# Optimization experiments

Measured on AMD Instinct MI355X. Metric: run time of the kernel, lower is better.

Reference implementation:

```python
import jax, jax.numpy as jnp
import numpy as np

B, S, D, H, E, K, F = 1, 1024, 1024, 16, 8, 2, 4096


def setup_inputs() -> dict:
    key = jax.random.key(0)
    ks = jax.random.split(key, 8)
    n = lambda k, shape, sc: (jax.random.normal(k, shape, dtype=jnp.float32) * sc)
    return {
        "x": n(ks[0], (B, S, D), 1.0),
        "w_qkv": n(ks[1], (D, 3 * D), D ** -0.5),
        "w_o": n(ks[2], (D, D), D ** -0.5),
        "g1": jnp.ones((D,), jnp.float32),
        "b1": jnp.zeros((D,), jnp.float32),
        "wg": n(ks[3], (D, E), D ** -0.5),
        "w1": n(ks[4], (E, D, F), D ** -0.5),
        "bb1": jnp.zeros((E, F), jnp.float32),
        "w2": n(ks[5], (E, F, D), F ** -0.5),
        "bb2": jnp.zeros((E, D), jnp.float32),
        "g2": jnp.ones((D,), jnp.float32),
        "b2": jnp.zeros((D,), jnp.float32),
    }


def layernorm(x, g, b, eps=1e-5):
    m = x.mean(-1, keepdims=True)
    v = ((x - m) ** 2).mean(-1, keepdims=True)
    return (x - m) * jax.lax.rsqrt(v + eps) * g + b


def reference(x, w_qkv, w_o, g1, b1, wg, w1, bb1, w2, bb2, g2, b2):
    b, s, d = x.shape
    hd = d // H
    # --- multi-head causal self-attention ---
    qkv = x @ w_qkv  # [b,s,3d]
    q, k, v = jnp.split(qkv, 3, axis=-1)
    to_heads = lambda t: t.reshape(b, s, H, hd).transpose(0, 2, 1, 3)  # [b,h,s,hd]
    q, k, v = to_heads(q), to_heads(k), to_heads(v)
    scores = jnp.einsum("bhqd,bhkd->bhqk", q, k) / jnp.sqrt(jnp.float32(hd))
    causal = jnp.tril(jnp.ones((s, s), bool))
    scores = jnp.where(causal, scores, jnp.finfo(scores.dtype).min)
    attn = jax.nn.softmax(scores, axis=-1)
    o = jnp.einsum("bhqk,bhkd->bhqd", attn, v)
    o = o.transpose(0, 2, 1, 3).reshape(b, s, d) @ w_o
    # --- add & norm ---
    h = layernorm(x + o, g1, b1)
    # --- MoE FFN: softmax router, top-k, renormalized combine ---
    probs = jax.nn.softmax(h @ wg, axis=-1)  # [b,s,E]
    topv, topi = jax.lax.top_k(probs, K)
    topv = topv / topv.sum(-1, keepdims=True)
    w = (topv[..., None] * jax.nn.one_hot(topi, E, dtype=h.dtype)).sum(-2)  # [b,s,E]
    h1 = jax.nn.gelu(jnp.einsum("bsd,edf->ebsf", h, w1) + bb1[:, None, None, :])
    y = jnp.einsum("ebsf,efd->ebsd", h1, w2) + bb2[:, None, None, :]
    moe = jnp.einsum("ebsd,bse->bsd", y, w)
    # --- residual + norm of MoE block ---
    return layernorm(h + moe, g2, b2)
```

## Files before the change

kernel.cpp:

```cpp
#include <hip/hip_runtime.h>
#include <hip/hip_bf16.h>
#include <math.h>

#define SEQ 1024
#define DIM 1024
#define NH  16
#define NE  8
#define FF  4096

typedef float f32x4 __attribute__((ext_vector_type(4)));
typedef short short8 __attribute__((ext_vector_type(8)));
typedef short s16x4 __attribute__((ext_vector_type(4)));

#define WAIT_VM(N) asm volatile("s_waitcnt vmcnt(" #N ")" ::: "memory")

__device__ __forceinline__ ushort f2bf(float f) {
  union { float f; unsigned u; } v; v.f = f;
  unsigned r = v.u + 0x7FFF + ((v.u >> 16) & 1);
  return (ushort)(r >> 16);
}
__device__ __forceinline__ float bf2f(ushort h) {
  union { unsigned u; float f; } v; v.u = ((unsigned)h) << 16;
  return v.f;
}

__device__ __forceinline__ float gelu_tanh(float x) {
  return 0.5f * x * (1.f + tanhf(0.7978845608028654f * (x + 0.044715f * x * x * x)));
}
__device__ __forceinline__ float gelu_fast(float x) {
  float u = 1.5957691216057308f * (x + 0.044715f * x * x * x);
  return x / (1.f + __expf(-u));
}

__device__ __forceinline__ void gl2lds16(const void* g, void* l) {
  __builtin_amdgcn_global_load_lds(
      (const __attribute__((address_space(1))) unsigned int*)g,
      (__attribute__((address_space(3))) unsigned int*)l, 16, 0, 0);
}

__global__ __launch_bounds__(256) void wconv_kernel(
    const float* __restrict__ w1, const float* __restrict__ w2,
    const float* __restrict__ wq, const float* __restrict__ wo,
    ushort* __restrict__ w1T, ushort* __restrict__ w2T,
    ushort* __restrict__ wqT, ushort* __restrict__ wqTl,
    ushort* __restrict__ woT, ushort* __restrict__ woTl) {
  __shared__ __align__(16) ushort th[64 * 64];
  __shared__ __align__(16) ushort tl[64 * 64];
  int z = blockIdx.z, t = threadIdx.x;
  const float* src; ushort* dh; ushort* dl = nullptr; int R, C, r0, c0;
  if (z < 8) {
    src = w1 + (size_t)z * DIM * FF;  dh = w1T + (size_t)z * FF * DIM;
    R = DIM; C = FF; r0 = blockIdx.y * 64; c0 = blockIdx.x * 64;
  } else if (z < 16) {
    src = w2 + (size_t)(z - 8) * FF * DIM;  dh = w2T + (size_t)(z - 8) * DIM * FF;
    R = FF; C = DIM; r0 = blockIdx.x * 64; c0 = blockIdx.y * 64;
  } else if (z == 16) {
    if (blockIdx.x >= 48) return;
    src = wq; dh = wqT; dl = wqTl;
    R = DIM; C = 3 * DIM; r0 = blockIdx.y * 64; c0 = blockIdx.x * 64;
  } else {
    if (blockIdx.x >= 16) return;
    src = wo; dh = woT; dl = woTl;
    R = DIM; C = DIM; r0 = blockIdx.y * 64; c0 = blockIdx.x * 64;
  }
  int ry = (t >> 4) * 4;
  int cx = (t & 15) * 4;
  f32x4 v[4];
#pragma unroll
  for (int j = 0; j < 4; j++)
    v[j] = *(const f32x4*)&src[(size_t)(r0 + ry + j) * C + c0 + cx];
#pragma unroll
  for (int i = 0; i < 4; i++) {
    int trow = cx + i;
    int o = trow * 64 + (((ry >> 3) ^ (trow & 7)) << 3) + (ry & 7);
    ushort uh[4], ul[4];
#pragma unroll
    for (int j = 0; j < 4; j++) {
      float f = v[j][i];
      ushort hh = f2bf(f);
      uh[j] = hh;
      if (dl) ul[j] = f2bf(f - bf2f(hh));
    }
    *(s16x4*)&th[o] = *(const s16x4*)uh;
    if (dl) *(s16x4*)&tl[o] = *(const s16x4*)ul;
  }
  __syncthreads();
  int tr = t >> 2, tc = (t & 3) * 16;
  int b0 = (tc >> 3) ^ (tr & 7);
  int b1 = ((tc >> 3) + 1) ^ (tr & 7);
  short8 u0 = *(const short8*)&th[tr * 64 + b0 * 8];
  short8 u1 = *(const short8*)&th[tr * 64 + b1 * 8];
  size_t dbase = (size_t)(c0 + tr) * R + r0 + tc;
  *(short8*)&dh[dbase] = u0;
  *(short8*)&dh[dbase + 8] = u1;
  if (dl) {
    short8 l0 = *(const short8*)&tl[tr * 64 + b0 * 8];
    short8 l1 = *(const short8*)&tl[tr * 64 + b1 * 8];
    *(short8*)&dl[dbase] = l0;
    *(short8*)&dl[dbase + 8] = l1;
  }
}

__global__ __launch_bounds__(256) void bfsplit_kernel(const float* __restrict__ in,
                                                      ushort* __restrict__ oh,
                                                      ushort* __restrict__ ol) {
  int i = (blockIdx.x * 256 + threadIdx.x) * 4;
  f32x4 v = *(const f32x4*)&in[i];
  ushort h[4], l[4];
#pragma unroll
  for (int j = 0; j < 4; j++) { h[j] = f2bf(v[j]); l[j] = f2bf(v[j] - bf2f(h[j])); }
  *(s16x4*)&oh[i] = *(const s16x4*)h;
  *(s16x4*)&ol[i] = *(const s16x4*)l;
}

template <int EPI, int KSPLIT>
__global__ __launch_bounds__(256) void mm_fast(
    const ushort* __restrict__ A, const ushort* __restrict__ BT,
    const float* __restrict__ bias, void* __restrict__ Cout,
    const int* __restrict__ tok, const int* __restrict__ offcnt,
    int N, int K)
{
  int zz = blockIdx.z;
  int e  = (KSPLIT > 1) ? (zz & (NE - 1)) : zz;
  int ks = (KSPLIT > 1) ? (zz >> 3) : 0;
  int off = offcnt[e], cnt = offcnt[NE + e];
  int m0 = blockIdx.y * 128;
  if (m0 >= cnt) return;
  int n0 = blockIdx.x * 128;
  const ushort* Bp = BT + (size_t)e * N * K;
  const int Kc = K / KSPLIT;
  const int kbase = ks * Kc;

  __shared__ __align__(16) ushort As[2][128 * 32];
  __shared__ __align__(16) ushort Bs[2][128 * 32];

  int t = threadIdx.x, lane = t & 63, w = t >> 6, wr = w >> 1, wc = w & 1;

  const ushort* aG[2]; const ushort* bG[2];
  int lofs[2];
#pragma unroll
  for (int c = 0; c < 2; c++) {
    int gid = w * 128 + c * 64 + lane;
    int m = gid >> 2, p = gid & 3;
    int kg = p ^ ((m >> 1) & 3);
    int mc = m0 + m; if (mc > cnt - 1) mc = cnt - 1;
    int arow = tok ? tok[off + mc] : (off + mc);
    aG[c] = A + (size_t)arow * K + kbase + kg * 8;
    bG[c] = Bp + (size_t)(n0 + m) * K + kbase + kg * 8;
    lofs[c] = (w * 128 + c * 64) * 8;
  }

  int aro[4], bro[4];
#pragma unroll
  for (int mi = 0; mi < 4; mi++) {
    int m = wr * 64 + mi * 16 + (lane & 15);
    aro[mi] = (m * 4 + ((lane >> 4) ^ ((m >> 1) & 3))) * 8;
  }
#pragma unroll
  for (int ni = 0; ni < 4; ni++) {
    int n = wc * 64 + ni * 16 + (lane & 15);
    bro[ni] = (n * 4 + ((lane >> 4) ^ ((n >> 1) & 3))) * 8;
  }

  f32x4 acc[4][4] = {};
  const int nt = Kc / 32;

#pragma unroll
  for (int c = 0; c < 2; c++) { gl2lds16(aG[c], &As[0][lofs[c]]); gl2lds16(bG[c], &Bs[0][lofs[c]]); }
  if (nt > 1) {
#pragma unroll
    for (int c = 0; c < 2; c++) { gl2lds16(aG[c] + 32, &As[1][lofs[c]]); gl2lds16(bG[c] + 32, &Bs[1][lofs[c]]); }
  }

  for (int tt = 0; tt < nt; tt++) {
    if (tt + 1 < nt) WAIT_VM(4); else WAIT_VM(0);
    __builtin_amdgcn_s_barrier();
    int b = tt & 1;
    short8 af[4], bf[4];
#pragma unroll
    for (int mi = 0; mi < 4; mi++) af[mi] = *(const short8*)&As[b][aro[mi]];
#pragma unroll
    for (int ni = 0; ni < 4; ni++) bf[ni] = *(const short8*)&Bs[b][bro[ni]];
#pragma unroll
    for (int mi = 0; mi < 4; mi++)
#pragma unroll
      for (int ni = 0; ni < 4; ni++)
        acc[mi][ni] = __builtin_amdgcn_mfma_f32_16x16x32_bf16(af[mi], bf[ni], acc[mi][ni], 0, 0, 0);
    asm volatile("s_waitcnt lgkmcnt(0)" ::: "memory");
    __builtin_amdgcn_sched_barrier(0);
    __builtin_amdgcn_s_barrier();
    if (tt + 2 < nt) {
      int ko = (tt + 2) * 32;
#pragma unroll
      for (int c = 0; c < 2; c++) { gl2lds16(aG[c] + ko, &As[b][lofs[c]]); gl2lds16(bG[c] + ko, &Bs[b][lofs[c]]); }
    }
  }

  const float* biasp = (EPI == 3) ? nullptr : bias + (size_t)e * N;
  float* Cp = (float*)Cout + (size_t)ks * 2048 * N;
#pragma unroll
  for (int mi = 0; mi < 4; mi++) {
#pragma unroll
    for (int j = 0; j < 4; j++) {
      int grow = m0 + wr * 64 + mi * 16 + (lane >> 4) * 4 + j;
      if (grow >= cnt) continue;
      size_t rbase = (size_t)(off + grow) * N;
#pragma unroll
      for (int ni = 0; ni < 4; ni++) {
        int gcol = n0 + wc * 64 + ni * 16 + (lane & 15);
        float v = acc[mi][ni][j];
        if (EPI == 1) ((ushort*)Cout)[rbase + gcol] = f2bf(gelu_fast(v + biasp[gcol]));
        else if (EPI == 2) ((float*)Cout)[rbase + gcol] = v + biasp[gcol];
        else Cp[rbase + gcol] = v;
      }
    }
  }
}

__global__ __launch_bounds__(256) void mm_split(
    const ushort* __restrict__ Ah, const ushort* __restrict__ Al,
    const ushort* __restrict__ Bh, const ushort* __restrict__ Bl,
    float* __restrict__ C, int N, int K)
{
  int m0 = blockIdx.y * 128;
  int n0 = blockIdx.x * 128;

  __shared__ __align__(16) ushort Ahs[2][4096], Als[2][4096];
  __shared__ __align__(16) ushort Bhs[2][4096], Bls[2][4096];

  int t = threadIdx.x, lane = t & 63, w = t >> 6, wr = w >> 1, wc = w & 1;

  const ushort *aGh[2], *aGl[2], *bGh[2], *bGl[2];
  int lofs[2];
#pragma unroll
  for (int c = 0; c < 2; c++) {
    int gid = w * 128 + c * 64 + lane;
    int m = gid >> 2, p = gid & 3;
    int kg = p ^ ((m >> 1) & 3);
    aGh[c] = Ah + (size_t)(m0 + m) * K + kg * 8;
    aGl[c] = Al + (size_t)(m0 + m) * K + kg * 8;
    bGh[c] = Bh + (size_t)(n0 + m) * K + kg * 8;
    bGl[c] = Bl + (size_t)(n0 + m) * K + kg * 8;
    lofs[c] = (w * 128 + c * 64) * 8;
  }

  int aro[4], bro[4];
#pragma unroll
  for (int mi = 0; mi < 4; mi++) {
    int m = wr * 64 + mi * 16 + (lane & 15);
    aro[mi] = (m * 4 + ((lane >> 4) ^ ((m >> 1) & 3))) * 8;
  }
#pragma unroll
  for (int ni = 0; ni < 4; ni++) {
    int n = wc * 64 + ni * 16 + (lane & 15);
    bro[ni] = (n * 4 + ((lane >> 4) ^ ((n >> 1) & 3))) * 8;
  }

  f32x4 acc[4][4] = {};
  const int nt = K / 32;

#pragma unroll
  for (int c = 0; c < 2; c++) {
    gl2lds16(aGh[c], &Ahs[0][lofs[c]]); gl2lds16(aGl[c], &Als[0][lofs[c]]);
    gl2lds16(bGh[c], &Bhs[0][lofs[c]]); gl2lds16(bGl[c], &Bls[0][lofs[c]]);
  }
  if (nt > 1) {
#pragma unroll
    for (int c = 0; c < 2; c++) {
      gl2lds16(aGh[c] + 32, &Ahs[1][lofs[c]]); gl2lds16(aGl[c] + 32, &Als[1][lofs[c]]);
      gl2lds16(bGh[c] + 32, &Bhs[1][lofs[c]]); gl2lds16(bGl[c] + 32, &Bls[1][lofs[c]]);
    }
  }

  for (int tt = 0; tt < nt; tt++) {
    if (tt + 1 < nt) WAIT_VM(8); else WAIT_VM(0);
    __builtin_amdgcn_s_barrier();
    int b = tt & 1;
    short8 ah[4], al_[4], bh[4], bl_[4];
#pragma unroll
    for (int mi = 0; mi < 4; mi++) {
      ah[mi] = *(const short8*)&Ahs[b][aro[mi]];
      al_[mi] = *(const short8*)&Als[b][aro[mi]];
    }
#pragma unroll
    for (int ni = 0; ni < 4; ni++) {
      bh[ni] = *(const short8*)&Bhs[b][bro[ni]];
      bl_[ni] = *(const short8*)&Bls[b][bro[ni]];
    }
#pragma unroll
    for (int mi = 0; mi < 4; mi++)
#pragma unroll
      for (int ni = 0; ni < 4; ni++) {
        acc[mi][ni] = __builtin_amdgcn_mfma_f32_16x16x32_bf16(al_[mi], bh[ni], acc[mi][ni], 0, 0, 0);
        acc[mi][ni] = __builtin_amdgcn_mfma_f32_16x16x32_bf16(ah[mi], bl_[ni], acc[mi][ni], 0, 0, 0);
        acc[mi][ni] = __builtin_amdgcn_mfma_f32_16x16x32_bf16(ah[mi], bh[ni], acc[mi][ni], 0, 0, 0);
      }
    asm volatile("s_waitcnt lgkmcnt(0)" ::: "memory");
    __builtin_amdgcn_sched_barrier(0);
    __builtin_amdgcn_s_barrier();
    if (tt + 2 < nt) {
      int ko = (tt + 2) * 32;
#pragma unroll
      for (int c = 0; c < 2; c++) {
        gl2lds16(aGh[c] + ko, &Ahs[b][lofs[c]]); gl2lds16(aGl[c] + ko, &Als[b][lofs[c]]);
        gl2lds16(bGh[c] + ko, &Bhs[b][lofs[c]]); gl2lds16(bGl[c] + ko, &Bls[b][lofs[c]]);
      }
    }
  }

#pragma unroll
  for (int mi = 0; mi < 4; mi++)
#pragma unroll
    for (int j = 0; j < 4; j++) {
      int grow = m0 + wr * 64 + mi * 16 + (lane >> 4) * 4 + j;
      size_t rbase = (size_t)grow * N;
#pragma unroll
      for (int ni = 0; ni < 4; ni++) {
        int gcol = n0 + wc * 64 + ni * 16 + (lane & 15);
        C[rbase + gcol] = acc[mi][ni][j];
      }
    }
}

template <int EPI, int SPLIT>
__global__ __launch_bounds__(256) void mm_bf16(
    const float* __restrict__ A, const float* __restrict__ B,
    const float* __restrict__ bias, float* __restrict__ C,
    const int* __restrict__ tok, const int* __restrict__ offcnt,
    int M, int N, int K)
{
  int e = blockIdx.z;
  int off = 0, cnt = M;
  if (offcnt) { off = offcnt[e]; cnt = offcnt[NE + e]; }
  int m0 = blockIdx.y * 128;
  if (m0 >= cnt) return;
  const float* Bp = B + (size_t)e * K * N;
  const float* biasp = (EPI == 0) ? nullptr : bias + (size_t)e * N;
  int n0 = blockIdx.x * 128;

  __shared__ __align__(16) ushort As[(SPLIT + 1) * 128 * 32];
  __shared__ __align__(16) ushort Bs[(SPLIT + 1) * 128 * 32];

  int t = threadIdx.x;
  int lane = t & 63;
  int w = t >> 6, wr = w >> 1, wc = w & 1;

  const float* aptr[2];
  int aws[2];
  for (int i = 0; i < 2; i++) {
    int mr = i * 64 + (t >> 2);
    int mc = m0 + mr; if (mc > cnt - 1) mc = cnt - 1;
    int arow = tok ? tok[off + mc] : (off + mc);
    aptr[i] = A + (size_t)arow * K + (t & 3) * 8;
    aws[i] = mr * 32 + (t & 3) * 8;
  }

  int bn = t >> 1, bkh = (t & 1) * 16;
  const float* bptr = Bp + (size_t)bkh * N + n0 + bn;
  int bws0 = bn * 32 + 8 * (((bkh >> 3) + 0) ^ (bn & 3));
  int bws1 = bn * 32 + 8 * (((bkh >> 3) + 1) ^ (bn & 3));

  int aro[4], bro[4];
#pragma unroll
  for (int mi = 0; mi < 4; mi++)
    aro[mi] = (wr * 64 + mi * 16 + (lane & 15)) * 32 + (lane >> 4) * 8;
#pragma unroll
  for (int ni = 0; ni < 4; ni++) {
    int n = wc * 64 + ni * 16 + (lane & 15);
    bro[ni] = n * 32 + 8 * ((lane >> 4) ^ (n & 3));
  }

  f32x4 acc[4][4] = {};

  for (int k0 = 0; k0 < K; k0 += 32) {
#pragma unroll
    for (int i = 0; i < 2; i++) {
      f32x4 v0 = *(const f32x4*)(aptr[i] + k0);
      f32x4 v1 = *(const f32x4*)(aptr[i] + k0 + 4);
      ushort uh[8], ul[8];
#pragma unroll
      for (int j = 0; j < 4; j++) {
        float f0 = v0[j], f1 = v1[j];
        ushort h0 = f2bf(f0), h1 = f2bf(f1);
        uh[j] = h0; uh[4 + j] = h1;
        if (SPLIT) { ul[j] = f2bf(f0 - bf2f(h0)); ul[4 + j] = f2bf(f1 - bf2f(h1)); }
      }
      *(short8*)&As[aws[i]] = *(const short8*)uh;
      if (SPLIT) *(short8*)&As[4096 + aws[i]] = *(const short8*)ul;
    }
    {
      const float* bp = bptr + (size_t)k0 * N;
      ushort uh[16], ul[16];
#pragma unroll
      for (int i = 0; i < 16; i++) {
        float f = bp[(size_t)i * N];
        ushort h = f2bf(f);
        uh[i] = h;
        if (SPLIT) ul[i] = f2bf(f - bf2f(h));
      }
      *(short8*)&Bs[bws0] = *(const short8*)&uh[0];
      *(short8*)&Bs[bws1] = *(const short8*)&uh[8];
      if (SPLIT) {
        *(short8*)&Bs[4096 + bws0] = *(const short8*)&ul[0];
        *(short8*)&Bs[4096 + bws1] = *(const short8*)&ul[8];
      }
    }
    __syncthreads();
    short8 afh[4], bfh[4], afl[4], bfl[4];
#pragma unroll
    for (int mi = 0; mi < 4; mi++) {
      afh[mi] = *(const short8*)&As[aro[mi]];
      if (SPLIT) afl[mi] = *(const short8*)&As[4096 + aro[mi]];
    }
#pragma unroll
    for (int ni = 0; ni < 4; ni++) {
      bfh[ni] = *(const short8*)&Bs[bro[ni]];
      if (SPLIT) bfl[ni] = *(const short8*)&Bs[4096 + bro[ni]];
    }
#pragma unroll
    for (int mi = 0; mi < 4; mi++)
#pragma unroll
      for (int ni = 0; ni < 4; ni++) {
        if (SPLIT) {
          acc[mi][ni] = __builtin_amdgcn_mfma_f32_16x16x32_bf16(afl[mi], bfh[ni], acc[mi][ni], 0, 0, 0);
          acc[mi][ni] = __builtin_amdgcn_mfma_f32_16x16x32_bf16(afh[mi], bfl[ni], acc[mi][ni], 0, 0, 0);
        }
        acc[mi][ni] = __builtin_amdgcn_mfma_f32_16x16x32_bf16(afh[mi], bfh[ni], acc[mi][ni], 0, 0, 0);
      }
    __syncthreads();
  }

#pragma unroll
  for (int mi = 0; mi < 4; mi++) {
#pragma unroll
    for (int j = 0; j < 4; j++) {
      int grow = m0 + wr * 64 + mi * 16 + (lane >> 4) * 4 + j;
      if (grow >= cnt) continue;
      size_t rbase = (size_t)(off + grow) * N;
#pragma unroll
      for (int ni = 0; ni < 4; ni++) {
        int gcol = n0 + wc * 64 + ni * 16 + (lane & 15);
        float v = acc[mi][ni][j];
        if (EPI >= 1) v += biasp[gcol];
        if (EPI == 1) v = gelu_tanh(v);
        C[rbase + gcol] = v;
      }
    }
  }
}

__device__ __forceinline__ int vidx(int d, int key) {
  return d * 64 + ((((key >> 3) ^ (d & 7)) << 3) | (key & 7));
}

__global__ __launch_bounds__(256, 1) void attn_mfma(const float* __restrict__ qkv,
                                                    float* __restrict__ o) {
  const int qb = blockIdx.x;
  const int head = blockIdx.y;
  const int q0 = qb * 128;
  const int t = threadIdx.x;
  const int lane = t & 63, w = t >> 6;
  const int g = lane >> 4, l4 = lane & 15;

  __shared__ __align__(16) ushort Kh[64 * 64], Kl[64 * 64];
  __shared__ __align__(16) ushort Vh[64 * 64], Vl[64 * 64];
  __shared__ __align__(16) ushort Ph[4][32 * 72], Pl[4][32 * 72];

  short8 qh[2][2], ql[2][2];
#pragma unroll
  for (int mi = 0; mi < 2; mi++)
#pragma unroll
    for (int ks = 0; ks < 2; ks++) {
      int row = q0 + w * 32 + mi * 16 + l4;
      const float* qp = qkv + (size_t)row * 3072 + head * 64 + ks * 32 + g * 8;
      f32x4 a = *(const f32x4*)qp;
      f32x4 b4 = *(const f32x4*)(qp + 4);
      ushort uh[8], ul_[8];
#pragma unroll
      for (int j = 0; j < 4; j++) {
        ushort h0 = f2bf(a[j]), h1 = f2bf(b4[j]);
        uh[j] = h0; uh[4 + j] = h1;
        ul_[j] = f2bf(a[j] - bf2f(h0)); ul_[4 + j] = f2bf(b4[j] - bf2f(h1));
      }
      qh[mi][ks] = *(const short8*)uh;
      ql[mi][ks] = *(const short8*)ul_;
    }

  float m_s[2][4], l_s[2][4];
  f32x4 O[2][4] = {};
#pragma unroll
  for (int mi = 0; mi < 2; mi++)
#pragma unroll
    for (int j = 0; j < 4; j++) { m_s[mi][j] = -INFINITY; l_s[mi][j] = 0.f; }

  const int nt = 2 * (qb + 1);
  for (int kt = 0; kt < nt; kt++) {
    const int kv0 = kt * 64;
    __syncthreads();
    {
      int key = t >> 2;
      int dblk = (t & 3) * 16;
      const float* kp = qkv + (size_t)(kv0 + key) * 3072 + 1024 + head * 64 + dblk;
      const float* vp = kp + 1024;
      f32x4 k0 = *(const f32x4*)kp, k1 = *(const f32x4*)(kp + 4),
            k2 = *(const f32x4*)(kp + 8), k3 = *(const f32x4*)(kp + 12);
      f32x4 v0 = *(const f32x4*)vp, v1 = *(const f32x4*)(vp + 4),
            v2 = *(const f32x4*)(vp + 8), v3 = *(const f32x4*)(vp + 12);
      float kf[16] = {k0[0],k0[1],k0[2],k0[3], k1[0],k1[1],k1[2],k1[3],
                      k2[0],k2[1],k2[2],k2[3], k3[0],k3[1],k3[2],k3[3]};
      float vf[16] = {v0[0],v0[1],v0[2],v0[3], v1[0],v1[1],v1[2],v1[3],
                      v2[0],v2[1],v2[2],v2[3], v3[0],v3[1],v3[2],v3[3]};
#pragma unroll
      for (int half = 0; half < 2; half++) {
        int d8 = (dblk >> 3) + half;
        int idx = key * 64 + ((d8 ^ (key & 7)) << 3);
        ushort uh[8], ul_[8];
#pragma unroll
        for (int j = 0; j < 8; j++) {
          float f = kf[half * 8 + j];
          ushort h = f2bf(f);
          uh[j] = h; ul_[j] = f2bf(f - bf2f(h));
        }
        *(short8*)&Kh[idx] = *(const short8*)uh;
        *(short8*)&Kl[idx] = *(const short8*)ul_;
      }
#pragma unroll
      for (int i = 0; i < 16; i++) {
        int d = dblk + i;
        int idx = vidx(d, key);
        float f = vf[i];
        ushort h = f2bf(f);
        Vh[idx] = h; Vl[idx] = f2bf(f - bf2f(h));
      }
    }
    __syncthreads();

    if (kv0 <= q0 + w * 32 + 31) {
      f32x4 S[2][4] = {};
#pragma unroll
      for (int ks = 0; ks < 2; ks++) {
        short8 kbh[4], kbl[4];
#pragma unroll
        for (int ni = 0; ni < 4; ni++) {
          int key = ni * 16 + l4;
          int d8 = ks * 4 + g;
          int idx = key * 64 + ((d8 ^ (key & 7)) << 3);
          kbh[ni] = *(const short8*)&Kh[idx];
          kbl[ni] = *(const short8*)&Kl[idx];
        }
#pragma unroll
        for (int mi = 0; mi < 2; mi++)
#pragma unroll
          for (int ni = 0; ni < 4; ni++) {
            S[mi][ni] = __builtin_amdgcn_mfma_f32_16x16x32_bf16(ql[mi][ks], kbh[ni], S[mi][ni], 0, 0, 0);
            S[mi][ni] = __builtin_amdgcn_mfma_f32_16x16x32_bf16(qh[mi][ks], kbl[ni], S[mi][ni], 0, 0, 0);
            S[mi][ni] = __builtin_amdgcn_mfma_f32_16x16x32_bf16(qh[mi][ks], kbh[ni], S[mi][ni], 0, 0, 0);
          }
      }
#pragma unroll
      for (int mi = 0; mi < 2; mi++) {
        int rowb = q0 + w * 32 + mi * 16 + g * 4;
        float mx[4] = {-INFINITY, -INFINITY, -INFINITY, -INFINITY};
#pragma unroll
        for (int ni = 0; ni < 4; ni++) {
          int col = kv0 + ni * 16 + l4;
#pragma unroll
          for (int j = 0; j < 4; j++) {
            float s = S[mi][ni][j] * 0.125f;
            if (col > rowb + j) s = -INFINITY;
            S[mi][ni][j] = s;
            mx[j] = fmaxf(mx[j], s);
          }
        }
#pragma unroll
        for (int j = 0; j < 4; j++) {
#pragma unroll
          for (int msk = 8; msk; msk >>= 1) mx[j] = fmaxf(mx[j], __shfl_xor(mx[j], msk));
          float mn = fmaxf(m_s[mi][j], mx[j]);
          float sc = __expf(m_s[mi][j] - mn);
          m_s[mi][j] = mn;
          l_s[mi][j] *= sc;
#pragma unroll
          for (int df = 0; df < 4; df++) O[mi][df][j] *= sc;
        }
        float ps[4] = {0.f, 0.f, 0.f, 0.f};
#pragma unroll
        for (int ni = 0; ni < 4; ni++)
#pragma unroll
          for (int j = 0; j < 4; j++) {
            float p = __expf(S[mi][ni][j] - m_s[mi][j]);
            ps[j] += p;
            int rl = mi * 16 + g * 4 + j, cl = ni * 16 + l4;
            ushort h = f2bf(p);
            Ph[w][rl * 72 + cl] = h;
            Pl[w][rl * 72 + cl] = f2bf(p - bf2f(h));
          }
#pragma unroll
        for (int j = 0; j < 4; j++) {
#pragma unroll
          for (int msk = 8; msk; msk >>= 1) ps[j] += __shfl_xor(ps[j], msk);
          l_s[mi][j] += ps[j];
        }
      }
      asm volatile("s_waitcnt lgkmcnt(0)" ::: "memory");
      __builtin_amdgcn_sched_barrier(0);
#pragma unroll
      for (int ks = 0; ks < 2; ks++) {
        short8 pah[2], pal[2], vbh[4], vbl[4];
#pragma unroll
        for (int mi = 0; mi < 2; mi++) {
          int idx = (mi * 16 + l4) * 72 + ks * 32 + g * 8;
          pah[mi] = *(const short8*)&Ph[w][idx];
          pal[mi] = *(const short8*)&Pl[w][idx];
        }
#pragma unroll
        for (int df = 0; df < 4; df++) {
          int d = df * 16 + l4;
          int k8 = ks * 4 + g;
          int idx = d * 64 + ((k8 ^ (d & 7)) << 3);
          vbh[df] = *(const short8*)&Vh[idx];
          vbl[df] = *(const short8*)&Vl[idx];
        }
#pragma unroll
        for (int mi = 0; mi < 2; mi++)
#pragma unroll
          for (int df = 0; df < 4; df++) {
            O[mi][df] = __builtin_amdgcn_mfma_f32_16x16x32_bf16(pal[mi], vbh[df], O[mi][df], 0, 0, 0);
            O[mi][df] = __builtin_amdgcn_mfma_f32_16x16x32_bf16(pah[mi], vbl[df], O[mi][df], 0, 0, 0);
            O[mi][df] = __builtin_amdgcn_mfma_f32_16x16x32_bf16(pah[mi], vbh[df], O[mi][df], 0, 0, 0);
          }
      }
    }
  }

#pragma unroll
  for (int mi = 0; mi < 2; mi++)
#pragma unroll
    for (int j = 0; j < 4; j++) {
      int row = q0 + w * 32 + mi * 16 + g * 4 + j;
      float inv = 1.f / l_s[mi][j];
#pragma unroll
      for (int df = 0; df < 4; df++)
        o[(size_t)row * DIM + head * 64 + df * 16 + l4] = O[mi][df][j] * inv;
    }
}

__device__ float block_reduce_256(float v, float* red, int t) {
  red[t] = v; __syncthreads();
  for (int st = 128; st > 0; st >>= 1) {
    if (t < st) red[t] += red[t + st];
    __syncthreads();
  }
  float r = red[0];
  __syncthreads();
  return r;
}

__global__ __launch_bounds__(256) void addln_kernel(const float* __restrict__ x,
                                                    const float* __restrict__ r,
                                                    const float* __restrict__ g,
                                                    const float* __restrict__ b,
                                                    float* __restrict__ out,
                                                    ushort* __restrict__ outb) {
  __shared__ float red[256];
  int row = blockIdx.x, t = threadIdx.x;
  float vals[4];
  float s = 0.f;
  for (int i = 0; i < 4; i++) {
    int d = t + i * 256;
    vals[i] = x[(size_t)row * DIM + d] + r[(size_t)row * DIM + d];
    s += vals[i];
  }
  float mean = block_reduce_256(s, red, t) * (1.f / DIM);
  float vs = 0.f;
  for (int i = 0; i < 4; i++) { float d = vals[i] - mean; vs += d * d; }
  float var = block_reduce_256(vs, red, t) * (1.f / DIM);
  float inv = rsqrtf(var + 1e-5f);
  for (int i = 0; i < 4; i++) {
    int d = t + i * 256;
    float v = (vals[i] - mean) * inv * g[d] + b[d];
    out[(size_t)row * DIM + d] = v;
    if (outb) outb[(size_t)row * DIM + d] = f2bf(v);
  }
}

__global__ __launch_bounds__(256) void router_kernel(const float* __restrict__ h,
                                                     const float* __restrict__ wg,
                                                     int* __restrict__ topi,
                                                     float* __restrict__ topw) {
  __shared__ float red[NE][256];
  int tkn = blockIdx.x, t = threadIdx.x;
  float acc[NE] = {};
  for (int i = 0; i < 4; i++) {
    int d = t + i * 256;
    float hv = h[(size_t)tkn * DIM + d];
    const float* wr = wg + (size_t)d * NE;
    for (int e = 0; e < NE; e++) acc[e] += hv * wr[e];
  }
  for (int e = 0; e < NE; e++) red[e][t] = acc[e];
  __syncthreads();
  for (int st = 128; st > 0; st >>= 1) {
    if (t < st)
      for (int e = 0; e < NE; e++) red[e][t] += red[e][t + st];
    __syncthreads();
  }
  if (t == 0) {
    float l[NE];
    for (int e = 0; e < NE; e++) l[e] = red[e][0];
    int i0 = 0;
    for (int e = 1; e < NE; e++) if (l[e] > l[i0]) i0 = e;
    int i1 = -1;
    for (int e = 0; e < NE; e++) {
      if (e == i0) continue;
      if (i1 < 0 || l[e] > l[i1]) i1 = e;
    }
    float p1 = __expf(l[i1] - l[i0]);
    float inv = 1.f / (1.f + p1);
    topi[tkn * 2] = i0; topi[tkn * 2 + 1] = i1;
    topw[tkn * 2] = inv; topw[tkn * 2 + 1] = p1 * inv;
  }
}

__global__ __launch_bounds__(1024) void compact_kernel(const int* __restrict__ topi,
                                                       int* __restrict__ tok,
                                                       int* __restrict__ assign_row,
                                                       int* __restrict__ offcnt) {
  __shared__ int scan[1024];
  __shared__ int sbase;
  int t = threadIdx.x;
  if (t == 0) sbase = 0;
  __syncthreads();
  for (int e = 0; e < NE; e++) {
    int which = -1;
    if (topi[t * 2] == e) which = 0;
    else if (topi[t * 2 + 1] == e) which = 1;
    scan[t] = (which >= 0) ? 1 : 0;
    __syncthreads();
    for (int s2 = 1; s2 < 1024; s2 <<= 1) {
      int add = (t >= s2) ? scan[t - s2] : 0;
      __syncthreads();
      scan[t] += add;
      __syncthreads();
    }
    int incl = scan[t];
    int total = scan[1023];
    int base = sbase;
    if (which >= 0) {
      int pos = base + incl - 1;
      tok[pos] = t;
      assign_row[t * 2 + which] = pos;
    }
    if (t == 0) { offcnt[e] = base; offcnt[NE + e] = total; }
    __syncthreads();
    if (t == 0) sbase = base + total;
    __syncthreads();
  }
}

template <int KS>
__global__ __launch_bounds__(256) void final_ln_kernel(const float* __restrict__ h,
                                                       const float* __restrict__ y,
                                                       const int* __restrict__ assign_row,
                                                       const float* __restrict__ topw,
                                                       const int* __restrict__ topi,
                                                       const float* __restrict__ bb2,
                                                       const float* __restrict__ g,
                                                       const float* __restrict__ b,
                                                       float* __restrict__ out) {
  __shared__ float red[256];
  int row = blockIdx.x, t = threadIdx.x;
  int r0 = assign_row[row * 2], r1 = assign_row[row * 2 + 1];
  float w0 = topw[row * 2], w1 = topw[row * 2 + 1];
  float vals[4];
  float s = 0.f;
  for (int i = 0; i < 4; i++) {
    int d = t + i * 256;
    float acc0 = 0.f, acc1 = 0.f;
#pragma unroll
    for (int p = 0; p < KS; p++) {
      acc0 += y[(size_t)p * 2048 * DIM + (size_t)r0 * DIM + d];
      acc1 += y[(size_t)p * 2048 * DIM + (size_t)r1 * DIM + d];
    }
    float v = h[(size_t)row * DIM + d] + w0 * acc0 + w1 * acc1;
    if (KS > 1) {
      int e0 = topi[row * 2], e1 = topi[row * 2 + 1];
      v += w0 * bb2[e0 * DIM + d] + w1 * bb2[e1 * DIM + d];
    }
    vals[i] = v;
    s += v;
  }
  float mean = block_reduce_256(s, red, t) * (1.f / DIM);
  float vs = 0.f;
  for (int i = 0; i < 4; i++) { float d = vals[i] - mean; vs += d * d; }
  float var = block_reduce_256(vs, red, t) * (1.f / DIM);
  float inv = rsqrtf(var + 1e-5f);
  for (int i = 0; i < 4; i++) {
    int d = t + i * 256;
    out[(size_t)row * DIM + d] = (vals[i] - mean) * inv * g[d] + b[d];
  }
}

extern "C" void kernel_launch(void* const* d_in, const int* in_sizes, int n_in,
                              void* d_out, int out_size, void* d_ws, size_t ws_size,
                              hipStream_t stream) {
  const float* x     = (const float*)d_in[0];
  const float* w_qkv = (const float*)d_in[1];
  const float* w_o   = (const float*)d_in[2];
  const float* g1    = (const float*)d_in[3];
  const float* b1    = (const float*)d_in[4];
  const float* wg    = (const float*)d_in[5];
  const float* w1    = (const float*)d_in[6];
  const float* bb1   = (const float*)d_in[7];
  const float* w2    = (const float*)d_in[8];
  const float* bb2   = (const float*)d_in[9];
  const float* g2    = (const float*)d_in[10];
  const float* b2    = (const float*)d_in[11];
  float* out = (float*)d_out;
  float* ws = (float*)d_ws;

  const bool fast = ws_size >= (size_t)46671872 * 4;

  if (fast) {
    float* qkv    = ws;
    float* attn_o = ws + 3145728;
    float* oproj  = ws + 4194304;
    float* h      = ws + 5242880;
    float* ybuf   = ws + 6291456;
    float* topw   = ws + 8388608;
    int*   ibase  = (int*)(ws + 8390656);
    int* topi       = ibase;
    int* tok        = ibase + 2048;
    int* assign_row = ibase + 4096;
    int* offcnt     = ibase + 6144;
    ushort* hb  = (ushort*)(ws + 8398848);
    ushort* h1b = (ushort*)(ws + 8923136);
    ushort* w1T = (ushort*)(ws + 13117440);
    ushort* w2T = (ushort*)(ws + 29894656);
    ushort* wqT  = h1b;
    ushort* wqTl = h1b + 3145728;
    ushort* woT  = h1b + 6291456;
    ushort* woTl = h1b + 7340032;
    ushort* xh = (ushort*)ybuf;
    ushort* xl = xh + 1048576;
    ushort* oh = xh + 2097152;
    ushort* ol = xh + 3145728;
    float* ypart = (float*)w1T;

    wconv_kernel<<<dim3(64, 16, 18), 256, 0, stream>>>(w1, w2, w_qkv, w_o,
                                                       w1T, w2T, wqT, wqTl, woT, woTl);
    bfsplit_kernel<<<dim3(SEQ * DIM / 1024), 256, 0, stream>>>(x, xh, xl);
    mm_split<<<dim3(24, 8), 256, 0, stream>>>(xh, xl, wqT, wqTl, qkv, 3 * DIM, DIM);
    attn_mfma<<<dim3(8, NH), 256, 0, stream>>>(qkv, attn_o);
    bfsplit_kernel<<<dim3(SEQ * DIM / 1024), 256, 0, stream>>>(attn_o, oh, ol);
    mm_split<<<dim3(8, 8), 256, 0, stream>>>(oh, ol, woT, woTl, oproj, DIM, DIM);
    addln_kernel<<<dim3(SEQ), 256, 0, stream>>>(x, oproj, g1, b1, h, hb);
    router_kernel<<<dim3(SEQ), 256, 0, stream>>>(h, wg, topi, topw);
    compact_kernel<<<dim3(1), 1024, 0, stream>>>(topi, tok, assign_row, offcnt);
    mm_fast<1, 1><<<dim3(FF / 128, 8, NE), 256, 0, stream>>>(hb, w1T, bb1, (void*)h1b,
                                                             tok, offcnt, FF, DIM);
    mm_fast<3, 4><<<dim3(DIM / 128, 8, NE * 4), 256, 0, stream>>>(h1b, w2T, nullptr,
                                                                  (void*)ypart,
                                                                  nullptr, offcnt, DIM, FF);
    final_ln_kernel<4><<<dim3(SEQ), 256, 0, stream>>>(h, ypart, assign_row, topw,
                                                      topi, bb2, g2, b2, out);
  } else {
    float* qkv    = ws;
    float* attn_o = ws + 3145728;
    float* oproj  = ws + 4194304;
    float* h      = ws + 5242880;
    float* h1     = ws + 6291456;
    float* ybuf   = ws + 14680064;
    float* topw   = ws + 16777216;
    int*   ibase  = (int*)(ws + 16779264);
    int* topi       = ibase;
    int* tok        = ibase + 2048;
    int* assign_row = ibase + 4096;
    int* offcnt     = ibase + 6144;

    mm_bf16<0, 1><<<dim3(24, 8, 1), 256, 0, stream>>>(x, w_qkv, nullptr, qkv,
                                                      nullptr, nullptr, SEQ, 3 * DIM, DIM);
    attn_mfma<<<dim3(8, NH), 256, 0, stream>>>(qkv, attn_o);
    mm_bf16<0, 1><<<dim3(8, 8, 1), 256, 0, stream>>>(attn_o, w_o, nullptr, oproj,
                                                     nullptr, nullptr, SEQ, DIM, DIM);
    addln_kernel<<<dim3(SEQ), 256, 0, stream>>>(x, oproj, g1, b1, h, nullptr);
    router_kernel<<<dim3(SEQ), 256, 0, stream>>>(h, wg, topi, topw);
    compact_kernel<<<dim3(1), 1024, 0, stream>>>(topi, tok, assign_row, offcnt);
    mm_bf16<1, 0><<<dim3(32, 8, NE), 256, 0, stream>>>(h, w1, bb1, h1,
                                                       tok, offcnt, SEQ, FF, DIM);
    mm_bf16<2, 0><<<dim3(8, 8, NE), 256, 0, stream>>>(h1, w2, bb2, ybuf,
                                                      nullptr, offcnt, SEQ, DIM, FF);
    final_ln_kernel<1><<<dim3(SEQ), 256, 0, stream>>>(h, ybuf, assign_row, topw,
                                                      nullptr, nullptr, g2, b2, out);
  }
}
```

Baseline: 369.7 us.

## Fuse fp32-to-bf16 expert weight conversion into MoE GEMM B-tile loads

Drops the separate transpose-and-convert pass over the w1/w2 expert weights (8x1024x4096 fp32 each) and has the MoE GEMM read fp32 weights directly, converting to bf16 while staging B tiles into a padded LDS layout. This removes a full read plus write of the converted weights and an extra kernel. In exchange, both GEMM operands now go through registers with plain loads instead of async global-to-LDS copies, and the pipeline is single-stage register prefetch. The GEMM also reads twice as many bytes per B element, and each expert tile is re-read by every M-block.

```diff
diff --git a/kernel.cpp b/kernel.cpp
--- a/kernel.cpp
+++ b/kernel.cpp
@@ -39,23 +39,14 @@
 }
 
 __global__ __launch_bounds__(256) void wconv_kernel(
-    const float* __restrict__ w1, const float* __restrict__ w2,
     const float* __restrict__ wq, const float* __restrict__ wo,
-    ushort* __restrict__ w1T, ushort* __restrict__ w2T,
     ushort* __restrict__ wqT, ushort* __restrict__ wqTl,
     ushort* __restrict__ woT, ushort* __restrict__ woTl) {
   __shared__ __align__(16) ushort th[64 * 64];
   __shared__ __align__(16) ushort tl[64 * 64];
   int z = blockIdx.z, t = threadIdx.x;
-  const float* src; ushort* dh; ushort* dl = nullptr; int R, C, r0, c0;
-  if (z < 8) {
-    src = w1 + (size_t)z * DIM * FF;  dh = w1T + (size_t)z * FF * DIM;
-    R = DIM; C = FF; r0 = blockIdx.y * 64; c0 = blockIdx.x * 64;
-  } else if (z < 16) {
-    src = w2 + (size_t)(z - 8) * FF * DIM;  dh = w2T + (size_t)(z - 8) * DIM * FF;
-    R = FF; C = DIM; r0 = blockIdx.x * 64; c0 = blockIdx.y * 64;
-  } else if (z == 16) {
-    if (blockIdx.x >= 48) return;
+  const float* src; ushort* dh; ushort* dl; int R, C, r0, c0;
+  if (z == 0) {
     src = wq; dh = wqT; dl = wqTl;
     R = DIM; C = 3 * DIM; r0 = blockIdx.y * 64; c0 = blockIdx.x * 64;
   } else {
@@ -79,26 +70,24 @@
       float f = v[j][i];
       ushort hh = f2bf(f);
       uh[j] = hh;
-      if (dl) ul[j] = f2bf(f - bf2f(hh));
+      ul[j] = f2bf(f - bf2f(hh));
     }
     *(s16x4*)&th[o] = *(const s16x4*)uh;
-    if (dl) *(s16x4*)&tl[o] = *(const s16x4*)ul;
+    *(s16x4*)&tl[o] = *(const s16x4*)ul;
   }
   __syncthreads();
   int tr = t >> 2, tc = (t & 3) * 16;
   int b0 = (tc >> 3) ^ (tr & 7);
   int b1 = ((tc >> 3) + 1) ^ (tr & 7);
+  size_t dbase = (size_t)(c0 + tr) * R + r0 + tc;
   short8 u0 = *(const short8*)&th[tr * 64 + b0 * 8];
   short8 u1 = *(const short8*)&th[tr * 64 + b1 * 8];
-  size_t dbase = (size_t)(c0 + tr) * R + r0 + tc;
   *(short8*)&dh[dbase] = u0;
   *(short8*)&dh[dbase + 8] = u1;
-  if (dl) {
-    short8 l0 = *(const short8*)&tl[tr * 64 + b0 * 8];
-    short8 l1 = *(const short8*)&tl[tr * 64 + b1 * 8];
-    *(short8*)&dl[dbase] = l0;
-    *(short8*)&dl[dbase + 8] = l1;
-  }
+  short8 l0 = *(const short8*)&tl[tr * 64 + b0 * 8];
+  short8 l1 = *(const short8*)&tl[tr * 64 + b1 * 8];
+  *(short8*)&dl[dbase] = l0;
+  *(short8*)&dl[dbase + 8] = l1;
 }
 
 __global__ __launch_bounds__(256) void bfsplit_kernel(const float* __restrict__ in,
@@ -114,8 +103,8 @@
 }
 
 template <int EPI, int KSPLIT>
-__global__ __launch_bounds__(256) void mm_fast(
-    const ushort* __restrict__ A, const ushort* __restrict__ BT,
+__global__ __launch_bounds__(256) void mm_fexp(
+    const ushort* __restrict__ A, const float* __restrict__ Bf,
     const float* __restrict__ bias, void* __restrict__ Cout,
     const int* __restrict__ tok, const int* __restrict__ offcnt,
     int N, int K)
@@ -127,17 +116,15 @@
   int m0 = blockIdx.y * 128;
   if (m0 >= cnt) return;
   int n0 = blockIdx.x * 128;
-  const ushort* Bp = BT + (size_t)e * N * K;
-  const int Kc = K / KSPLIT;
-  const int kbase = ks * Kc;
+  const float* Bp = Bf + (size_t)e * K * N;
+  const int Kc = K / KSPLIT, kbase = ks * Kc;
 
   __shared__ __align__(16) ushort As[2][128 * 32];
-  __shared__ __align__(16) ushort Bs[2][128 * 32];
+  __shared__ __align__(16) ushort Bs[2][128 * 40];
 
   int t = threadIdx.x, lane = t & 63, w = t >> 6, wr = w >> 1, wc = w & 1;
 
-  const ushort* aG[2]; const ushort* bG[2];
-  int lofs[2];
+  const ushort* aG[2]; int aw[2];
 #pragma unroll
   for (int c = 0; c < 2; c++) {
     int gid = w * 128 + c * 64 + lane;
@@ -146,9 +133,12 @@
     int mc = m0 + m; if (mc > cnt - 1) mc = cnt - 1;
     int arow = tok ? tok[off + mc] : (off + mc);
     aG[c] = A + (size_t)arow * K + kbase + kg * 8;
-    bG[c] = Bp + (size_t)(n0 + m) * K + kbase + kg * 8;
-    lofs[c] = (w * 128 + c * 64) * 8;
-  }
+    aw[c] = gid * 8;
+  }
+
+  int kb = t >> 5, nb = t & 31;
+  const float* bG = Bp + (size_t)(kbase + kb * 4) * N + n0 + nb * 4;
+  int bslot = kb ^ ((nb & 3) << 1);
 
   int aro[4], bro[4];
 #pragma unroll
@@ -159,41 +149,52 @@
 #pragma unroll
   for (int ni = 0; ni < 4; ni++) {
     int n = wc * 64 + ni * 16 + (lane & 15);
-    bro[ni] = (n * 4 + ((lane >> 4) ^ ((n >> 1) & 3))) * 8;
+    bro[ni] = n * 40 + ((((lane >> 4) * 2) ^ (((n >> 2) & 3) << 1))) * 4;
   }
 
   f32x4 acc[4][4] = {};
   const int nt = Kc / 32;
 
-#pragma unroll
-  for (int c = 0; c < 2; c++) { gl2lds16(aG[c], &As[0][lofs[c]]); gl2lds16(bG[c], &Bs[0][lofs[c]]); }
-  if (nt > 1) {
-#pragma unroll
-    for (int c = 0; c < 2; c++) { gl2lds16(aG[c] + 32, &As[1][lofs[c]]); gl2lds16(bG[c] + 32, &Bs[1][lofs[c]]); }
-  }
+  short8 ra0 = *(const short8*)aG[0];
+  short8 ra1 = *(const short8*)aG[1];
+  f32x4 rb0 = *(const f32x4*)(bG + (size_t)0 * N);
+  f32x4 rb1 = *(const f32x4*)(bG + (size_t)1 * N);
+  f32x4 rb2 = *(const f32x4*)(bG + (size_t)2 * N);
+  f32x4 rb3 = *(const f32x4*)(bG + (size_t)3 * N);
 
   for (int tt = 0; tt < nt; tt++) {
-    if (tt + 1 < nt) WAIT_VM(4); else WAIT_VM(0);
-    __builtin_amdgcn_s_barrier();
     int b = tt & 1;
-    short8 af[4], bf[4];
-#pragma unroll
-    for (int mi = 0; mi < 4; mi++) af[mi] = *(const short8*)&As[b][aro[mi]];
-#pragma unroll
-    for (int ni = 0; ni < 4; ni++) bf[ni] = *(const short8*)&Bs[b][bro[ni]];
-#pragma unroll
-    for (int mi = 0; mi < 4; mi++)
-#pragma unroll
-      for (int ni = 0; ni < 4; ni++)
-        acc[mi][ni] = __builtin_amdgcn_mfma_f32_16x16x32_bf16(af[mi], bf[ni], acc[mi][ni], 0, 0, 0);
+    *(short8*)&As[b][aw[0]] = ra0;
+    *(short8*)&As[b][aw[1]] = ra1;
+#pragma unroll
+    for (int i = 0; i < 4; i++) {
+      ushort u[4];
+      u[0] = f2bf(rb0[i]); u[1] = f2bf(rb1[i]);
+      u[2] = f2bf(rb2[i]); u[3] = f2bf(rb3[i]);
+      *(s16x4*)&Bs[b][(nb * 4 + i) * 40 + bslot * 4] = *(const s16x4*)u;
+    }
+    if (tt + 1 < nt) {
+      int ko = (tt + 1) * 32;
+      ra0 = *(const short8*)(aG[0] + ko);
+      ra1 = *(const short8*)(aG[1] + ko);
+      rb0 = *(const f32x4*)(bG + (size_t)(ko + 0) * N);
+      rb1 = *(const f32x4*)(bG + (size_t)(ko + 1) * N);
+      rb2 = *(const f32x4*)(bG + (size_t)(ko + 2) * N);
+      rb3 = *(const f32x4*)(bG + (size_t)(ko + 3) * N);
+    }
     asm volatile("s_waitcnt lgkmcnt(0)" ::: "memory");
     __builtin_amdgcn_sched_barrier(0);
     __builtin_amdgcn_s_barrier();
-    if (tt + 2 < nt) {
-      int ko = (tt + 2) * 32;
-#pragma unroll
-      for (int c = 0; c < 2; c++) { gl2lds16(aG[c] + ko, &As[b][lofs[c]]); gl2lds16(bG[c] + ko, &Bs[b][lofs[c]]); }
-    }
+    short8 af[4], bf[4];
+#pragma unroll
+    for (int mi = 0; mi < 4; mi++) af[mi] = *(const short8*)&As[b][aro[mi]];
+#pragma unroll
+    for (int ni = 0; ni < 4; ni++) bf[ni] = *(const short8*)&Bs[b][bro[ni]];
+#pragma unroll
+    for (int mi = 0; mi < 4; mi++)
+#pragma unroll
+      for (int ni = 0; ni < 4; ni++)
+        acc[mi][ni] = __builtin_amdgcn_mfma_f32_16x16x32_bf16(af[mi], bf[ni], acc[mi][ni], 0, 0, 0);
   }
 
   const float* biasp = (EPI == 3) ? nullptr : bias + (size_t)e * N;
@@ -210,8 +211,7 @@
         int gcol = n0 + wc * 64 + ni * 16 + (lane & 15);
         float v = acc[mi][ni][j];
         if (EPI == 1) ((ushort*)Cout)[rbase + gcol] = f2bf(gelu_fast(v + biasp[gcol]));
-        else if (EPI == 2) ((float*)Cout)[rbase + gcol] = v + biasp[gcol];
-        else Cp[rbase + gcol] = v;
+        else          Cp[rbase + gcol] = v;
       }
     }
   }
@@ -834,20 +834,18 @@
     int* offcnt     = ibase + 6144;
     ushort* hb  = (ushort*)(ws + 8398848);
     ushort* h1b = (ushort*)(ws + 8923136);
-    ushort* w1T = (ushort*)(ws + 13117440);
-    ushort* w2T = (ushort*)(ws + 29894656);
-    ushort* wqT  = h1b;
-    ushort* wqTl = h1b + 3145728;
-    ushort* woT  = h1b + 6291456;
-    ushort* woTl = h1b + 7340032;
+    ushort* wqT  = (ushort*)(ws + 13117440);
+    ushort* wqTl = wqT + 3145728;
+    ushort* woT  = wqT + 6291456;
+    ushort* woTl = wqT + 7340032;
+    float* ypart = ws + 17311744;
     ushort* xh = (ushort*)ybuf;
     ushort* xl = xh + 1048576;
     ushort* oh = xh + 2097152;
     ushort* ol = xh + 3145728;
-    float* ypart = (float*)w1T;
-
-    wconv_kernel<<<dim3(64, 16, 18), 256, 0, stream>>>(w1, w2, w_qkv, w_o,
-                                                       w1T, w2T, wqT, wqTl, woT, woTl);
+
+    wconv_kernel<<<dim3(48, 16, 2), 256, 0, stream>>>(w_qkv, w_o,
+                                                      wqT, wqTl, woT, woTl);
     bfsplit_kernel<<<dim3(SEQ * DIM / 1024), 256, 0, stream>>>(x, xh, xl);
     mm_split<<<dim3(24, 8), 256, 0, stream>>>(xh, xl, wqT, wqTl, qkv, 3 * DIM, DIM);
     attn_mfma<<<dim3(8, NH), 256, 0, stream>>>(qkv, attn_o);
@@ -856,9 +854,9 @@
     addln_kernel<<<dim3(SEQ), 256, 0, stream>>>(x, oproj, g1, b1, h, hb);
     router_kernel<<<dim3(SEQ), 256, 0, stream>>>(h, wg, topi, topw);
     compact_kernel<<<dim3(1), 1024, 0, stream>>>(topi, tok, assign_row, offcnt);
-    mm_fast<1, 1><<<dim3(FF / 128, 8, NE), 256, 0, stream>>>(hb, w1T, bb1, (void*)h1b,
+    mm_fexp<1, 1><<<dim3(FF / 128, 8, NE), 256, 0, stream>>>(hb, w1, bb1, (void*)h1b,
                                                              tok, offcnt, FF, DIM);
-    mm_fast<3, 4><<<dim3(DIM / 128, 8, NE * 4), 256, 0, stream>>>(h1b, w2T, nullptr,
+    mm_fexp<3, 4><<<dim3(DIM / 128, 8, NE * 4), 256, 0, stream>>>(h1b, w2, nullptr,
                                                                   (void*)ypart,
                                                                   nullptr, offcnt, DIM, FF);
     final_ln_kernel<4><<<dim3(SEQ), 256, 0, stream>>>(h, ypart, assign_row, topw,
```

New measurement: 338.7 us. 1.09x faster.
